# Kernel tuning notes

Hardware: AMD Instinct MI355X
Metric: run time of the kernel (lower is better)

Reference implementation:

```python
import jax, jax.numpy as jnp
import numpy as np

INF = 1e9
EPS = 1e-5

def layer_norm(x, g, b):
    mu = jnp.mean(x, axis=-1, keepdims=True)
    var = jnp.mean(jnp.square(x - mu), axis=-1, keepdims=True)
    return (x - mu) * jax.lax.rsqrt(var + EPS) * g + b

def setup_inputs() -> dict:
    key = jax.random.key(0)
    ks = jax.random.split(key, 12)
    B, S, N = 1, 512, 384
    c_in, c_hid, c_z, H = 64, 32, 128, 8
    d = c_hid * H
    sc = lambda fan: 1.0 / np.sqrt(fan)
    return {
        "m": jax.random.normal(ks[0], (B, S, N, c_in), jnp.float32),
        "z": jax.random.normal(ks[1], (B, N, N, c_z), jnp.float32),
        "mask": jnp.ones((B, N, N), jnp.float32),
        "gamma_m": jnp.ones((c_in,), jnp.float32),
        "beta_m": jnp.zeros((c_in,), jnp.float32),
        "gamma_z": jnp.ones((c_z,), jnp.float32),
        "beta_z": jnp.zeros((c_z,), jnp.float32),
        "w_z": jax.random.normal(ks[2], (c_z, H), jnp.float32) * sc(c_z),
        "b_z": jnp.zeros((H,), jnp.float32),
        "w_v": jax.random.normal(ks[3], (c_in, d), jnp.float32) * sc(c_in),
        "b_v": jnp.zeros((d,), jnp.float32),
        "w_g": jax.random.normal(ks[4], (c_in, d), jnp.float32) * sc(c_in),
        "b_g": jnp.zeros((d,), jnp.float32),
        "w_o": jax.random.normal(ks[5], (d, c_in), jnp.float32) * sc(d),
        "b_o": jnp.zeros((c_in,), jnp.float32),
    }

def reference(m, z, mask, gamma_m, beta_m, gamma_z, beta_z,
              w_z, b_z, w_v, b_v, w_g, b_g, w_o, b_o):
    B, S, N, c_in = m.shape
    H = w_z.shape[-1]
    C = w_v.shape[-1] // H
    # pair branch: LN -> linear -> [B,H,Nq,Nk] logits + mask bias -> softmax
    zn = layer_norm(z, gamma_z, beta_z)
    logits = jnp.einsum('bqkz,zh->bhqk', zn, w_z) + b_z[None, :, None, None]
    logits = logits + (INF * (mask - 1.0))[:, None, :, :]
    w = jax.nn.softmax(logits, axis=-1)                      # [B,H,Nq,Nk]
    # MSA branch: LN -> value / gate projections
    mn = layer_norm(m, gamma_m, beta_m)
    v = (mn @ w_v + b_v).reshape(B, S, N, H, C)              # [B,S,Nk,H,C]
    o = jnp.einsum('bhqk,bskhc->bsqhc', w, v)                # broadcast over S
    g = jax.nn.sigmoid(mn @ w_g + b_g).reshape(B, S, N, H, C)
    out = (o * g).reshape(B, S, N, H * C) @ w_o + b_o
    return out
```

## Files before the change

### kernel.cpp

```cpp
#include <hip/hip_runtime.h>
#include <hip/hip_bf16.h>

#define INFV 1e9f
#define EPSV 1e-5f

typedef unsigned short u16;
typedef unsigned int u32;
typedef __attribute__((ext_vector_type(8))) short short8;
typedef __attribute__((ext_vector_type(4))) float float4v;

__device__ __forceinline__ u16 f2us(float f) {
    u32 v;
    __builtin_memcpy(&v, &f, 4);
    u32 r = v + 0x7fffu + ((v >> 16) & 1u);
    return (u16)(r >> 16);
}

__device__ __forceinline__ float wred_sum(float x) {
    #pragma unroll
    for (int o = 32; o; o >>= 1) x += __shfl_xor(x, o);
    return x;
}
__device__ __forceinline__ float wred_max(float x) {
    #pragma unroll
    for (int o = 32; o; o >>= 1) x = fmaxf(x, __shfl_xor(x, o));
    return x;
}

__device__ __forceinline__ void gld16(const void* g, void* l) {
    __builtin_amdgcn_global_load_lds(
        (const __attribute__((address_space(1))) unsigned int*)g,
        (__attribute__((address_space(3))) unsigned int*)l,
        16, 0, 0);
}

__global__ __launch_bounds__(256) void k_prep_ln(
    const float* __restrict__ m, const float* __restrict__ gm, const float* __restrict__ bm,
    u16* __restrict__ mn,
    const float* __restrict__ wv, const float* __restrict__ wg,
    const float* __restrict__ wo, const float* __restrict__ wz,
    u16* __restrict__ wv_t, u16* __restrict__ wg_t,
    u16* __restrict__ wo_t, u16* __restrict__ wzT)
{
    if (blockIdx.x < 12288) {
        const int tid  = threadIdx.x;
        const int wid  = tid >> 6;
        const int lane = tid & 63;
        const int rloc = lane >> 4;
        const int c4   = (lane & 15) * 4;
        const int row  = blockIdx.x * 16 + wid * 4 + rloc;
        const float4 x = *(const float4*)(m + (size_t)row * 64 + c4);
        float s1 = x.x + x.y + x.z + x.w;
        float s2 = x.x * x.x + x.y * x.y + x.z * x.z + x.w * x.w;
        #pragma unroll
        for (int o = 8; o; o >>= 1) { s1 += __shfl_xor(s1, o); s2 += __shfl_xor(s2, o); }
        const float mean = s1 * (1.0f / 64.0f);
        const float var  = s2 * (1.0f / 64.0f) - mean * mean;
        const float rs   = rsqrtf(var + EPSV);
        const float4 g = *(const float4*)(gm + c4);
        const float4 b = *(const float4*)(bm + c4);
        uint2 pk;
        pk.x = (u32)f2us((x.x - mean) * rs * g.x + b.x) | ((u32)f2us((x.y - mean) * rs * g.y + b.y) << 16);
        pk.y = (u32)f2us((x.z - mean) * rs * g.z + b.z) | ((u32)f2us((x.w - mean) * rs * g.w + b.w) << 16);
        *(uint2*)(mn + (size_t)row * 64 + c4) = pk;
    } else {
        const int i = (blockIdx.x - 12288) * 256 + threadIdx.x;
        if (i < 16384) {
            const int n = i >> 6, k = i & 63;
            wv_t[i] = f2us(wv[(size_t)k * 256 + n]);
        } else if (i < 32768) {
            const int j = i - 16384, n = j >> 6, k = j & 63;
            wg_t[j] = f2us(wg[(size_t)k * 256 + n]);
        } else if (i < 49152) {
            const int j = i - 32768, n = j >> 8, k = j & 255;
            wo_t[j] = f2us(wo[(size_t)k * 64 + n]);
        } else if (i < 51200) {
            const int j = i - 49152, n = j >> 7, k = j & 127;
            wzT[j] = (n < 8) ? f2us(wz[(size_t)k * 8 + n]) : (u16)0;
        }
    }
}

__global__ __launch_bounds__(256) void k_vT(
    const u16* __restrict__ mn, const u16* __restrict__ wv_t, u16* __restrict__ vTf)
{
    const int tid  = threadIdx.x;
    const int wid  = tid >> 6;
    const int lane = tid & 63;
    const int lrow = lane & 15;
    const int lkg  = lane >> 4;
    const int s    = blockIdx.y;
    const int k0   = blockIdx.x * 64 + wid * 16;

    const int kt   = blockIdx.x * 2 + (wid >> 1);
    const int lkgc = (wid & 1) * 2 + (lkg >> 1);
    const int joff = (lkg & 1) * 4;

    const u16* mnk = mn + ((size_t)s * 384 + k0 + lrow) * 64;
    const short8 a0 = *(const short8*)(mnk + lkg * 8);
    const short8 a1 = *(const short8*)(mnk + 32 + lkg * 8);

    #pragma unroll
    for (int nt = 0; nt < 16; nt++) {
        const short8 b0 = *(const short8*)(wv_t + (size_t)(nt * 16 + lrow) * 64 + lkg * 8);
        const short8 b1 = *(const short8*)(wv_t + (size_t)(nt * 16 + lrow) * 64 + 32 + lkg * 8);
        float4v acc = (float4v){0.f, 0.f, 0.f, 0.f};
        acc = __builtin_amdgcn_mfma_f32_16x16x32_bf16(a0, b0, acc, 0, 0, 0);
        acc = __builtin_amdgcn_mfma_f32_16x16x32_bf16(a1, b1, acc, 0, 0, 0);
        uint2 pk;
        pk.x = (u32)f2us(acc[0]) | ((u32)f2us(acc[1]) << 16);
        pk.y = (u32)f2us(acc[2]) | ((u32)f2us(acc[3]) << 16);
        *(uint2*)(vTf + ((((size_t)s * 12 + kt) * 16 + nt) << 9)
                      + ((lkgc << 4) + lrow) * 8 + joff) = pk;
    }
}

__global__ __launch_bounds__(256) void k_logits2(
    const float* __restrict__ z, const float* __restrict__ mask,
    const float* __restrict__ gz, const float* __restrict__ bz,
    const u16* __restrict__ wzT, const float* __restrict__ bzb,
    float* __restrict__ wbuf)
{
    const int tid   = threadIdx.x;
    const int wid   = tid >> 6;
    const int lane  = tid & 63;
    const int lrow  = lane & 15;
    const int lkg   = lane >> 4;
    const int pair0 = (blockIdx.x * 4 + wid) * 16;

    float x[4][8];
    float s1 = 0.0f, s2 = 0.0f;
    #pragma unroll
    for (int ks = 0; ks < 4; ks++) {
        const float4* zp = (const float4*)(z + (size_t)(pair0 + lrow) * 128 + ks * 32 + lkg * 8);
        const float4 a = zp[0], b = zp[1];
        x[ks][0] = a.x; x[ks][1] = a.y; x[ks][2] = a.z; x[ks][3] = a.w;
        x[ks][4] = b.x; x[ks][5] = b.y; x[ks][6] = b.z; x[ks][7] = b.w;
        #pragma unroll
        for (int j = 0; j < 8; j++) { s1 += x[ks][j]; s2 += x[ks][j] * x[ks][j]; }
    }
    s1 += __shfl_xor(s1, 16); s1 += __shfl_xor(s1, 32);
    s2 += __shfl_xor(s2, 16); s2 += __shfl_xor(s2, 32);
    const float mean = s1 * (1.0f / 128.0f);
    const float var  = s2 * (1.0f / 128.0f) - mean * mean;
    const float rs   = rsqrtf(var + EPSV);

    float4v acc = (float4v){0.f, 0.f, 0.f, 0.f};
    #pragma unroll
    for (int ks = 0; ks < 4; ks++) {
        const int c0 = ks * 32 + lkg * 8;
        const float4 g0 = *(const float4*)(gz + c0);
        const float4 g1 = *(const float4*)(gz + c0 + 4);
        const float4 b0 = *(const float4*)(bz + c0);
        const float4 b1 = *(const float4*)(bz + c0 + 4);
        const float gv[8] = {g0.x, g0.y, g0.z, g0.w, g1.x, g1.y, g1.z, g1.w};
        const float bvv[8] = {b0.x, b0.y, b0.z, b0.w, b1.x, b1.y, b1.z, b1.w};
        short8 afr;
        #pragma unroll
        for (int j = 0; j < 8; j++)
            afr[j] = (short)f2us((x[ks][j] - mean) * rs * gv[j] + bvv[j]);
        const short8 bfr = *(const short8*)(wzT + (size_t)lrow * 128 + c0);
        acc = __builtin_amdgcn_mfma_f32_16x16x32_bf16(afr, bfr, acc, 0, 0, 0);
    }
    if (lrow < 8) {
        const float bzv = bzb[lrow];
        #pragma unroll
        for (int r = 0; r < 4; r++) {
            const int p = pair0 + lkg * 4 + r;
            const float mb = INFV * (mask[p] - 1.0f);
            wbuf[(size_t)lrow * 147456 + p] = acc[r] + bzv + mb;
        }
    }
}

__global__ __launch_bounds__(256) void k_softmax_f(
    const float* __restrict__ wbuf, u16* __restrict__ wbf)
{
    const int r = blockIdx.x * 4 + (threadIdx.x >> 6);
    const int lane = threadIdx.x & 63;
    const float* base = wbuf + (size_t)r * 384;
    float v[6];
    float mx = -1e30f;
    #pragma unroll
    for (int j = 0; j < 6; j++) {
        v[j] = base[lane + j * 64];
        mx = fmaxf(mx, v[j]);
    }
    mx = wred_max(mx);
    float s = 0.0f;
    #pragma unroll
    for (int j = 0; j < 6; j++) {
        v[j] = __expf(v[j] - mx);
        s += v[j];
    }
    s = wred_sum(s);
    const float inv = 1.0f / s;

    const int h  = r / 384;
    const int q  = r - h * 384;
    const int qb = q >> 5;
    const int mt = (q >> 4) & 1;
    const int lr = q & 15;
    #pragma unroll
    for (int j = 0; j < 6; j++) {
        const int k   = lane + j * 64;
        const int kt  = k >> 5;
        const int lkg = (k >> 3) & 3;
        const int jj  = k & 7;
        wbf[((((size_t)(qb * 8 + h) * 12 + kt) * 2 + mt) << 9) + ((lkg << 4) + lr) * 8 + jj]
            = f2us(v[j] * inv);
    }
}

__global__ __launch_bounds__(256) void k_softmax(
    const float* __restrict__ wbuf, u16* __restrict__ wb16)
{
    const int r = blockIdx.x * 4 + (threadIdx.x >> 6);
    const int lane = threadIdx.x & 63;
    const float* base = wbuf + (size_t)r * 384;
    float v[6];
    float mx = -1e30f;
    #pragma unroll
    for (int j = 0; j < 6; j++) {
        v[j] = base[lane + j * 64];
        mx = fmaxf(mx, v[j]);
    }
    mx = wred_max(mx);
    float s = 0.0f;
    #pragma unroll
    for (int j = 0; j < 6; j++) {
        v[j] = __expf(v[j] - mx);
        s += v[j];
    }
    s = wred_sum(s);
    const float inv = 1.0f / s;
    u16* ob = wb16 + (size_t)r * 384;
    #pragma unroll
    for (int j = 0; j < 6; j++) ob[lane + j * 64] = f2us(v[j] * inv);
}

__global__ __launch_bounds__(512, 4) void k_fused8(
    const u16* __restrict__ mn, const u16* __restrict__ vTf,
    const float* __restrict__ bv, const float* __restrict__ bg, const float* __restrict__ bo,
    const u16* __restrict__ wg_t, const u16* __restrict__ wo_t,
    const u16* __restrict__ wbf, float* __restrict__ out)
{
    __shared__ __align__(16) char smem[67584];
    u16* vtt = (u16*)smem;
    u16* og  = (u16*)smem;

    const int tid  = threadIdx.x;
    const int w    = tid >> 6;
    const int wq   = w >> 1;
    const int wh   = w & 1;
    const int lane = tid & 63;
    const int lrow = lane & 15;
    const int lkg  = lane >> 4;
    const int stg  = w * 2;

    const int bid  = blockIdx.x;
    const int xcd  = bid & 7;
    const int slot = bid >> 3;
    const int sdiv = slot / 3;
    const int q0   = (slot - sdiv * 3) * 128;
    const int s    = sdiv * 8 + xcd;

    const int qb = (q0 >> 5) + wq;

    float4v oacc[16];
    #pragma unroll
    for (int mt = 0; mt < 2; mt++)
        #pragma unroll
        for (int nt = 0; nt < 8; nt++) {
            const float b = bv[wh * 128 + nt * 16 + lrow];
            oacc[mt * 8 + nt] = (float4v){b, b, b, b};
        }

    const u16* vfs = vTf + (((size_t)s * 12) << 13);

    {
        const u16* gp = vfs + ((size_t)stg << 9) + lane * 8;
        u16* lp = vtt + stg * 512;
        gld16(gp, lp);
        gld16(gp + 512, lp + 512);
    }
    __syncthreads();

    for (int kt = 0; kt < 12; kt++) {
        const int cur = kt & 1;
        if (kt < 11) {
            const u16* gp = vfs + ((((size_t)(kt + 1) * 16) + stg) << 9) + lane * 8;
            u16* lp = vtt + (((cur ^ 1) * 16 + stg) * 512);
            gld16(gp, lp);
            gld16(gp + 512, lp + 512);
        }
        const u16* vb = vtt + cur * 8192;
        #pragma unroll
        for (int hl = 0; hl < 4; hl++) {
            const size_t abase = (((size_t)(qb * 8 + wh * 4 + hl) * 12 + kt) * 2) << 9;
            const short8 a0 = *(const short8*)(wbf + abase + lane * 8);
            const short8 a1 = *(const short8*)(wbf + abase + 512 + lane * 8);
            const short8 b0 = *(const short8*)(vb + ((wh * 8 + hl * 2) * 512) + lane * 8);
            const short8 b1 = *(const short8*)(vb + ((wh * 8 + hl * 2 + 1) * 512) + lane * 8);
            const int nt = hl * 2;
            oacc[nt]         = __builtin_amdgcn_mfma_f32_16x16x32_bf16(a0, b0, oacc[nt], 0, 0, 0);
            oacc[8 + nt]     = __builtin_amdgcn_mfma_f32_16x16x32_bf16(a1, b0, oacc[8 + nt], 0, 0, 0);
            oacc[nt + 1]     = __builtin_amdgcn_mfma_f32_16x16x32_bf16(a0, b1, oacc[nt + 1], 0, 0, 0);
            oacc[8 + nt + 1] = __builtin_amdgcn_mfma_f32_16x16x32_bf16(a1, b1, oacc[8 + nt + 1], 0, 0, 0);
        }
        __syncthreads();
    }

    {
        const u16* mnq = mn + ((size_t)s * 384 + q0 + wq * 32 + lrow) * 64;
        #pragma unroll
        for (int mt = 0; mt < 2; mt++) {
            const short8 a0 = *(const short8*)(mnq + mt * 1024 + lkg * 8);
            const short8 a1 = *(const short8*)(mnq + mt * 1024 + 32 + lkg * 8);
            #pragma unroll
            for (int nt = 0; nt < 8; nt++) {
                const int hc0 = wh * 128 + nt * 16;
                const float bgv = bg[hc0 + lrow];
                const short8 b0 = *(const short8*)(wg_t + (size_t)(hc0 + lrow) * 64 + lkg * 8);
                const short8 b1 = *(const short8*)(wg_t + (size_t)(hc0 + lrow) * 64 + 32 + lkg * 8);
                float4v gacc = (float4v){bgv, bgv, bgv, bgv};
                gacc = __builtin_amdgcn_mfma_f32_16x16x32_bf16(a0, b0, gacc, 0, 0, 0);
                gacc = __builtin_amdgcn_mfma_f32_16x16x32_bf16(a1, b1, gacc, 0, 0, 0);
                #pragma unroll
                for (int r = 0; r < 4; r++) {
                    const float sg = 1.0f / (1.0f + __expf(-gacc[r]));
                    og[(size_t)(wq * 32 + mt * 16 + lkg * 4 + r) * 264 + hc0 + lrow]
                        = f2us(oacc[mt * 8 + nt][r] * sg);
                }
            }
        }
    }
    __syncthreads();

    #pragma unroll
    for (int mt = 0; mt < 2; mt++) {
        short8 af[8];
        #pragma unroll
        for (int ks = 0; ks < 8; ks++)
            af[ks] = *(const short8*)&og[(size_t)(wq * 32 + mt * 16 + lrow) * 264 + ks * 32 + lkg * 8];
        #pragma unroll
        for (int ntl = 0; ntl < 2; ntl++) {
            const int nto = wh * 2 + ntl;
            const float bov = bo[nto * 16 + lrow];
            float4v fac = (float4v){bov, bov, bov, bov};
            #pragma unroll
            for (int ks = 0; ks < 8; ks++) {
                const short8 b = *(const short8*)(wo_t + (size_t)(nto * 16 + lrow) * 256 + ks * 32 + lkg * 8);
                fac = __builtin_amdgcn_mfma_f32_16x16x32_bf16(af[ks], b, fac, 0, 0, 0);
            }
            #pragma unroll
            for (int r = 0; r < 4; r++)
                out[((size_t)s * 384 + q0 + wq * 32 + mt * 16 + lkg * 4 + r) * 64 + nto * 16 + lrow]
                    = fac[r];
        }
    }
}

__global__ __launch_bounds__(256, 2) void k_fused4(
    const u16* __restrict__ mn,
    const float* __restrict__ bv, const float* __restrict__ bg, const float* __restrict__ bo,
    const u16* __restrict__ wv_t, const u16* __restrict__ wg_t, const u16* __restrict__ wo_t,
    const u16* __restrict__ wb16, float* __restrict__ out)
{
    __shared__ __align__(16) char smem[67584];
    u16* vtt = (u16*)smem;
    u16* og  = (u16*)smem;

    const int tid  = threadIdx.x;
    const int wid  = tid >> 6;
    const int lane = tid & 63;
    const int lrow = lane & 15;
    const int lkg  = lane >> 4;
    const int s    = blockIdx.y;
    const int q0   = blockIdx.x * 128;

    const int vmt  = wid & 1;
    const int vnt0 = (wid >> 1) * 8;

    float4v oacc[32];
    #pragma unroll
    for (int mt = 0; mt < 2; mt++)
        #pragma unroll
        for (int nt = 0; nt < 16; nt++) {
            const float b = bv[nt * 16 + lrow];
            oacc[mt * 16 + nt] = (float4v){b, b, b, b};
        }

    for (int kt = 0; kt < 12; kt++) {
        const int k0 = kt * 32;
        float4v vacc[8];
        #pragma unroll
        for (int nt = 0; nt < 8; nt++) vacc[nt] = (float4v){0.f, 0.f, 0.f, 0.f};
        const u16* mnk = mn + ((size_t)s * 384 + k0 + vmt * 16 + lrow) * 64;
        #pragma unroll
        for (int ks = 0; ks < 2; ks++) {
            const short8 a = *(const short8*)(mnk + ks * 32 + lkg * 8);
            #pragma unroll
            for (int nt = 0; nt < 8; nt++) {
                const short8 b = *(const short8*)(wv_t + (size_t)((vnt0 + nt) * 16 + lrow) * 64 + ks * 32 + lkg * 8);
                vacc[nt] = __builtin_amdgcn_mfma_f32_16x16x32_bf16(a, b, vacc[nt], 0, 0, 0);
            }
        }
        u16* vb = vtt + (size_t)(kt & 1) * 8192;
        const int kg8 = vmt * 2 + (lkg >> 1);
        const int ko  = (lkg & 1) * 4;
        #pragma unroll
        for (int nt = 0; nt < 8; nt++) {
            uint2 pk;
            pk.x = (u32)f2us(vacc[nt][0]) | ((u32)f2us(vacc[nt][1]) << 16);
            pk.y = (u32)f2us(vacc[nt][2]) | ((u32)f2us(vacc[nt][3]) << 16);
            *(uint2*)&vb[((size_t)kg8 * 256 + (vnt0 + nt) * 16 + lrow) * 8 + ko] = pk;
        }
        __syncthreads();

        short8 ah[2][8];
        #pragma unroll
        for (int mt = 0; mt < 2; mt++)
            #pragma unroll
            for (int h = 0; h < 8; h++)
                ah[mt][h] = *(const short8*)(wb16 + (size_t)h * 147456
                              + (size_t)(q0 + wid * 32 + mt * 16 + lrow) * 384 + k0 + lkg * 8);
        #pragma unroll
        for (int nt = 0; nt < 16; nt++) {
            const short8 b = *(const short8*)&vb[((size_t)lkg * 256 + nt * 16 + lrow) * 8];
            oacc[nt]      = __builtin_amdgcn_mfma_f32_16x16x32_bf16(ah[0][nt >> 1], b, oacc[nt], 0, 0, 0);
            oacc[16 + nt] = __builtin_amdgcn_mfma_f32_16x16x32_bf16(ah[1][nt >> 1], b, oacc[16 + nt], 0, 0, 0);
        }
    }
    __syncthreads();

    #pragma unroll
    for (int mt = 0; mt < 2; mt++) {
        const u16* mnq = mn + ((size_t)s * 384 + q0 + wid * 32 + mt * 16 + lrow) * 64;
        const short8 a0 = *(const short8*)(mnq + lkg * 8);
        const short8 a1 = *(const short8*)(mnq + 32 + lkg * 8);
        #pragma unroll
        for (int nt = 0; nt < 16; nt++) {
            const float bgv = bg[nt * 16 + lrow];
            float4v gacc = (float4v){bgv, bgv, bgv, bgv};
            const short8 b0 = *(const short8*)(wg_t + (size_t)(nt * 16 + lrow) * 64 + lkg * 8);
            const short8 b1 = *(const short8*)(wg_t + (size_t)(nt * 16 + lrow) * 64 + 32 + lkg * 8);
            gacc = __builtin_amdgcn_mfma_f32_16x16x32_bf16(a0, b0, gacc, 0, 0, 0);
            gacc = __builtin_amdgcn_mfma_f32_16x16x32_bf16(a1, b1, gacc, 0, 0, 0);
            #pragma unroll
            for (int r = 0; r < 4; r++) {
                const float sg = 1.0f / (1.0f + __expf(-gacc[r]));
                og[(size_t)(wid * 32 + mt * 16 + lkg * 4 + r) * 264 + nt * 16 + lrow]
                    = f2us(oacc[mt * 16 + nt][r] * sg);
            }
        }
    }
    __syncthreads();

    #pragma unroll
    for (int mt = 0; mt < 2; mt++) {
        short8 af[8];
        #pragma unroll
        for (int ks = 0; ks < 8; ks++)
            af[ks] = *(const short8*)&og[(size_t)(wid * 32 + mt * 16 + lrow) * 264 + ks * 32 + lkg * 8];
        #pragma unroll
        for (int nt = 0; nt < 4; nt++) {
            const float bov = bo[nt * 16 + lrow];
            float4v fac = (float4v){bov, bov, bov, bov};
            #pragma unroll
            for (int ks = 0; ks < 8; ks++) {
                const short8 b = *(const short8*)(wo_t + (size_t)(nt * 16 + lrow) * 256 + ks * 32 + lkg * 8);
                fac = __builtin_amdgcn_mfma_f32_16x16x32_bf16(af[ks], b, fac, 0, 0, 0);
            }
            #pragma unroll
            for (int r = 0; r < 4; r++)
                out[((size_t)s * 384 + q0 + wid * 32 + mt * 16 + lkg * 4 + r) * 64 + nt * 16 + lrow]
                    = fac[r];
        }
    }
}

extern "C" void kernel_launch(void* const* d_in, const int* in_sizes, int n_in,
                              void* d_out, int out_size, void* d_ws, size_t ws_size,
                              hipStream_t stream) {
    const float* m    = (const float*)d_in[0];
    const float* z    = (const float*)d_in[1];
    const float* mask = (const float*)d_in[2];
    const float* gm   = (const float*)d_in[3];
    const float* bm   = (const float*)d_in[4];
    const float* gz   = (const float*)d_in[5];
    const float* bz   = (const float*)d_in[6];
    const float* wz   = (const float*)d_in[7];
    const float* bzb  = (const float*)d_in[8];
    const float* wv   = (const float*)d_in[9];
    const float* bv   = (const float*)d_in[10];
    const float* wg   = (const float*)d_in[11];
    const float* bg   = (const float*)d_in[12];
    const float* wo   = (const float*)d_in[13];
    const float* bo   = (const float*)d_in[14];
    float* out = (float*)d_out;

    char* ws = (char*)d_ws;
    float* wbuf = (float*)ws;
    u16*  wb16  = (u16*)(ws + 4718592);
    u16*  mn    = (u16*)(ws + 7077888);
    u16*  wv_t  = (u16*)(ws + 32243712);
    u16*  wg_t  = (u16*)(ws + 32276480);
    u16*  wo_t  = (u16*)(ws + 32309248);
    u16*  wzT   = (u16*)(ws + 32342016);
    u16*  vTf   = (u16*)(ws + 32346112);

    const bool big = ws_size >= 133009408ull;

    k_prep_ln<<<12488, 256, 0, stream>>>(m, gm, bm, mn, wv, wg, wo, wz, wv_t, wg_t, wo_t, wzT);
    if (big)
        k_vT<<<dim3(6, 512), 256, 0, stream>>>(mn, wv_t, vTf);
    k_logits2<<<2304, 256, 0, stream>>>(z, mask, gz, bz, wzT, bzb, wbuf);
    if (big) {
        k_softmax_f<<<768, 256, 0, stream>>>(wbuf, wb16);
        k_fused8<<<1536, 512, 0, stream>>>(mn, vTf, bv, bg, bo, wg_t, wo_t, wb16, out);
    } else {
        k_softmax<<<768, 256, 0, stream>>>(wbuf, wb16);
        k_fused4<<<dim3(3, 512), 256, 0, stream>>>(mn, bv, bg, bo, wv_t, wg_t, wo_t, wb16, out);
    }
}
```

Before: 389.2 us.

## Coalesce softmax bf16 fragment writes via LDS and double k-tile V staging

The pair softmax now processes 16 query rows per block, with 16 lanes per row and vectorized float4 loads. It stages the normalized bf16 probabilities in LDS, then writes them out in the MFMA fragment layout as 16-byte coalesced stores instead of scattered 2-byte stores. The fused attention/gating kernel stages two key tiles of V per pipeline step, which halves the number of barrier-separated iterations. This uses the full double-buffered LDS allocation and adds register pressure in the softmax.

```diff
diff --git a/kernel.cpp b/kernel.cpp
--- a/kernel.cpp
+++ b/kernel.cpp
@@ -173,8 +173,63 @@
     }
 }
 
-__global__ __launch_bounds__(256) void k_softmax_f(
+__global__ __launch_bounds__(256) void k_softmax_f2(
     const float* __restrict__ wbuf, u16* __restrict__ wbf)
+{
+    __shared__ __align__(16) u16 lds[16 * 392];
+
+    const int tid  = threadIdx.x;
+    const int w    = tid >> 6;
+    const int lane = tid & 63;
+    const int rg   = lane >> 4;
+    const int l16  = lane & 15;
+
+    const int bx = blockIdx.x;
+    const int h  = bx & 7;
+    const int qm = bx >> 3;
+    const int qb = qm >> 1;
+    const int mt = qm & 1;
+    const int rb = w * 4 + rg;
+    const int q  = qb * 32 + mt * 16 + rb;
+
+    const float* base = wbuf + (size_t)h * 147456 + (size_t)q * 384 + l16 * 24;
+    float v[24];
+    float mx = -1e30f;
+    #pragma unroll
+    for (int i = 0; i < 6; i++) {
+        const float4 x = *(const float4*)(base + i * 4);
+        v[i * 4 + 0] = x.x; v[i * 4 + 1] = x.y; v[i * 4 + 2] = x.z; v[i * 4 + 3] = x.w;
+        mx = fmaxf(mx, fmaxf(fmaxf(x.x, x.y), fmaxf(x.z, x.w)));
+    }
+    #pragma unroll
+    for (int o = 8; o; o >>= 1) mx = fmaxf(mx, __shfl_xor(mx, o));
+    float s = 0.0f;
+    #pragma unroll
+    for (int i = 0; i < 24; i++) { v[i] = __expf(v[i] - mx); s += v[i]; }
+    #pragma unroll
+    for (int o = 8; o; o >>= 1) s += __shfl_xor(s, o);
+    const float inv = 1.0f / s;
+
+    u16* lp = lds + rb * 392 + l16 * 24;
+    #pragma unroll
+    for (int i = 0; i < 12; i++) {
+        const u32 pk = (u32)f2us(v[2 * i] * inv) | ((u32)f2us(v[2 * i + 1] * inv) << 16);
+        *(u32*)(lp + 2 * i) = pk;
+    }
+    __syncthreads();
+
+    const int lr  = lane & 15;
+    const int lkg = lane >> 4;
+    #pragma unroll
+    for (int j = 0; j < 3; j++) {
+        const int kt = w * 3 + j;
+        const short8 f = *(const short8*)(lds + lr * 392 + kt * 32 + lkg * 8);
+        *(short8*)(wbf + ((((size_t)(qb * 8 + h) * 12 + kt) * 2 + mt) << 9) + lane * 8) = f;
+    }
+}
+
+__global__ __launch_bounds__(256) void k_softmax(
+    const float* __restrict__ wbuf, u16* __restrict__ wb16)
 {
     const int r = blockIdx.x * 4 + (threadIdx.x >> 6);
     const int lane = threadIdx.x & 63;
@@ -195,51 +250,12 @@
     }
     s = wred_sum(s);
     const float inv = 1.0f / s;
-
-    const int h  = r / 384;
-    const int q  = r - h * 384;
-    const int qb = q >> 5;
-    const int mt = (q >> 4) & 1;
-    const int lr = q & 15;
-    #pragma unroll
-    for (int j = 0; j < 6; j++) {
-        const int k   = lane + j * 64;
-        const int kt  = k >> 5;
-        const int lkg = (k >> 3) & 3;
-        const int jj  = k & 7;
-        wbf[((((size_t)(qb * 8 + h) * 12 + kt) * 2 + mt) << 9) + ((lkg << 4) + lr) * 8 + jj]
-            = f2us(v[j] * inv);
-    }
-}
-
-__global__ __launch_bounds__(256) void k_softmax(
-    const float* __restrict__ wbuf, u16* __restrict__ wb16)
-{
-    const int r = blockIdx.x * 4 + (threadIdx.x >> 6);
-    const int lane = threadIdx.x & 63;
-    const float* base = wbuf + (size_t)r * 384;
-    float v[6];
-    float mx = -1e30f;
-    #pragma unroll
-    for (int j = 0; j < 6; j++) {
-        v[j] = base[lane + j * 64];
-        mx = fmaxf(mx, v[j]);
-    }
-    mx = wred_max(mx);
-    float s = 0.0f;
-    #pragma unroll
-    for (int j = 0; j < 6; j++) {
-        v[j] = __expf(v[j] - mx);
-        s += v[j];
-    }
-    s = wred_sum(s);
-    const float inv = 1.0f / s;
     u16* ob = wb16 + (size_t)r * 384;
     #pragma unroll
     for (int j = 0; j < 6; j++) ob[lane + j * 64] = f2us(v[j] * inv);
 }
 
-__global__ __launch_bounds__(512, 4) void k_fused8(
+__global__ __launch_bounds__(512, 4) void k_fused9(
     const u16* __restrict__ mn, const u16* __restrict__ vTf,
     const float* __restrict__ bv, const float* __restrict__ bg, const float* __restrict__ bo,
     const u16* __restrict__ wg_t, const u16* __restrict__ wo_t,
@@ -256,7 +272,7 @@
     const int lane = tid & 63;
     const int lrow = lane & 15;
     const int lkg  = lane >> 4;
-    const int stg  = w * 2;
+    const int stg  = w * 4;
 
     const int bid  = blockIdx.x;
     const int xcd  = bid & 7;
@@ -281,32 +297,36 @@
     {
         const u16* gp = vfs + ((size_t)stg << 9) + lane * 8;
         u16* lp = vtt + stg * 512;
-        gld16(gp, lp);
-        gld16(gp + 512, lp + 512);
+        #pragma unroll
+        for (int i = 0; i < 4; i++) gld16(gp + i * 512, lp + i * 512);
     }
     __syncthreads();
 
-    for (int kt = 0; kt < 12; kt++) {
-        const int cur = kt & 1;
-        if (kt < 11) {
-            const u16* gp = vfs + ((((size_t)(kt + 1) * 16) + stg) << 9) + lane * 8;
-            u16* lp = vtt + (((cur ^ 1) * 16 + stg) * 512);
-            gld16(gp, lp);
-            gld16(gp + 512, lp + 512);
-        }
-        const u16* vb = vtt + cur * 8192;
-        #pragma unroll
-        for (int hl = 0; hl < 4; hl++) {
-            const size_t abase = (((size_t)(qb * 8 + wh * 4 + hl) * 12 + kt) * 2) << 9;
-            const short8 a0 = *(const short8*)(wbf + abase + lane * 8);
-            const short8 a1 = *(const short8*)(wbf + abase + 512 + lane * 8);
-            const short8 b0 = *(const short8*)(vb + ((wh * 8 + hl * 2) * 512) + lane * 8);
-            const short8 b1 = *(const short8*)(vb + ((wh * 8 + hl * 2 + 1) * 512) + lane * 8);
-            const int nt = hl * 2;
-            oacc[nt]         = __builtin_amdgcn_mfma_f32_16x16x32_bf16(a0, b0, oacc[nt], 0, 0, 0);
-            oacc[8 + nt]     = __builtin_amdgcn_mfma_f32_16x16x32_bf16(a1, b0, oacc[8 + nt], 0, 0, 0);
-            oacc[nt + 1]     = __builtin_amdgcn_mfma_f32_16x16x32_bf16(a0, b1, oacc[nt + 1], 0, 0, 0);
-            oacc[8 + nt + 1] = __builtin_amdgcn_mfma_f32_16x16x32_bf16(a1, b1, oacc[8 + nt + 1], 0, 0, 0);
+    for (int pt = 0; pt < 6; pt++) {
+        const int cur = pt & 1;
+        if (pt < 5) {
+            const u16* gp = vfs + ((size_t)((pt + 1) * 32 + stg) << 9) + lane * 8;
+            u16* lp = vtt + ((cur ^ 1) * 32 + stg) * 512;
+            #pragma unroll
+            for (int i = 0; i < 4; i++) gld16(gp + i * 512, lp + i * 512);
+        }
+        #pragma unroll 1
+        for (int sub = 0; sub < 2; sub++) {
+            const int kt = pt * 2 + sub;
+            const u16* vb = vtt + (cur * 32 + sub * 16) * 512;
+            #pragma unroll
+            for (int hl = 0; hl < 4; hl++) {
+                const size_t abase = (((size_t)(qb * 8 + wh * 4 + hl) * 12 + kt) * 2) << 9;
+                const short8 a0 = *(const short8*)(wbf + abase + lane * 8);
+                const short8 a1 = *(const short8*)(wbf + abase + 512 + lane * 8);
+                const short8 b0 = *(const short8*)(vb + ((wh * 8 + hl * 2) * 512) + lane * 8);
+                const short8 b1 = *(const short8*)(vb + ((wh * 8 + hl * 2 + 1) * 512) + lane * 8);
+                const int nt = hl * 2;
+                oacc[nt]         = __builtin_amdgcn_mfma_f32_16x16x32_bf16(a0, b0, oacc[nt], 0, 0, 0);
+                oacc[8 + nt]     = __builtin_amdgcn_mfma_f32_16x16x32_bf16(a1, b0, oacc[8 + nt], 0, 0, 0);
+                oacc[nt + 1]     = __builtin_amdgcn_mfma_f32_16x16x32_bf16(a0, b1, oacc[nt + 1], 0, 0, 0);
+                oacc[8 + nt + 1] = __builtin_amdgcn_mfma_f32_16x16x32_bf16(a1, b1, oacc[8 + nt + 1], 0, 0, 0);
+            }
         }
         __syncthreads();
     }
@@ -517,8 +537,8 @@
         k_vT<<<dim3(6, 512), 256, 0, stream>>>(mn, wv_t, vTf);
     k_logits2<<<2304, 256, 0, stream>>>(z, mask, gz, bz, wzT, bzb, wbuf);
     if (big) {
-        k_softmax_f<<<768, 256, 0, stream>>>(wbuf, wb16);
-        k_fused8<<<1536, 512, 0, stream>>>(mn, vTf, bv, bg, bo, wg_t, wo_t, wb16, out);
+        k_softmax_f2<<<192, 256, 0, stream>>>(wbuf, wb16);
+        k_fused9<<<1536, 512, 0, stream>>>(mn, vTf, bv, bg, bo, wg_t, wo_t, wb16, out);
     } else {
         k_softmax<<<768, 256, 0, stream>>>(wbuf, wb16);
         k_fused4<<<dim3(3, 512), 256, 0, stream>>>(mn, bv, bg, bo, wv_t, wg_t, wo_t, wb16, out);
```

New measurement: 386.9 us. No clear change (-0.6%).
